# Kernel optimization log

Hardware: AMD Instinct MI355X
Metric: run time of the kernel (lower is better)

## Reference

```python
import jax, jax.numpy as jnp
import numpy as np

NM = 4096; NP = 4096; EM = 65536; EP = 65536; H = 256; HEADS = 4; G = 32


def _lin(k, din, dout):
    k1, k2 = jax.random.split(k)
    return (jax.random.normal(k1, (din, dout), jnp.float32) * (1.0 / np.sqrt(din)),
            jax.random.normal(k2, (dout,), jnp.float32) * 0.01)


def setup_inputs() -> dict:
    key = jax.random.key(0)
    ks = jax.random.split(key, 32)
    inp = {}
    inp['x_mol'] = jax.random.normal(ks[0], (NM, 8), jnp.float32)
    inp['x_prot'] = jax.random.normal(ks[1], (NP, 4), jnp.float32)
    inp['ea_mol'] = jax.random.normal(ks[2], (EM, 2), jnp.float32)
    inp['ea_prot'] = jax.random.normal(ks[3], (EP, 2), jnp.float32)
    inp['ei_mol'] = jax.random.randint(ks[4], (2, EM), 0, NM)
    inp['ei_prot'] = jax.random.randint(ks[5], (2, EP), 0, NP)
    inp['batch_mol'] = jnp.sort(jax.random.randint(ks[6], (NM,), 0, G))
    inp['batch_prot'] = jnp.sort(jax.random.randint(ks[7], (NP,), 0, G))
    inp['node_lin_mol_w'], inp['node_lin_mol_b'] = _lin(ks[8], 8, H)
    inp['node_lin_prot_w'], inp['node_lin_prot_b'] = _lin(ks[9], 4, H)
    inp['edge_lin_mol_w'], inp['edge_lin_mol_b'] = _lin(ks[10], 2, H)
    inp['edge_lin_prot_w'], inp['edge_lin_prot_b'] = _lin(ks[11], 2, H)
    # two GINE conv layers per graph, each with a 2-layer MLP; stack layer dim first
    for pref, base in (('mol', 12), ('prot', 16)):
        w1 = []; b1 = []; w2 = []; b2 = []
        for l in range(2):
            w, b = _lin(ks[base + 2 * l], H, H); w1.append(w); b1.append(b)
            w, b = _lin(ks[base + 2 * l + 1], H, H); w2.append(w); b2.append(b)
        inp[pref + '_w1'] = jnp.stack(w1); inp[pref + '_b1'] = jnp.stack(b1)
        inp[pref + '_w2'] = jnp.stack(w2); inp[pref + '_b2'] = jnp.stack(b2)
    for pref, base in (('mp', 20), ('pm', 23)):
        inp[pref + '_wq'], inp[pref + '_bq'] = _lin(ks[base], H, H)
        inp[pref + '_wk'], inp[pref + '_bk'] = _lin(ks[base + 1], H, H)
        inp[pref + '_wv'], inp[pref + '_bv'] = _lin(ks[base + 2], H, H)
    inp['fc1_w'], inp['fc1_b'] = _lin(ks[26], 2 * H, H)
    inp['fc2_w'], inp['fc2_b'] = _lin(ks[27], H, 1)
    return inp


def _gine_stack(x, ei, e, w1, b1, w2, b2):
    # GINEConv (eps=0): x_i' = relu(nn(x_i + sum_j relu(x_j + e_ji))), 2 layers, shared edge emb
    src, dst = ei[0], ei[1]
    n = x.shape[0]
    for l in range(w1.shape[0]):
        msg = jax.nn.relu(x[src] + e)                      # [E, H]
        agg = jax.ops.segment_sum(msg, dst, num_segments=n)  # [N, H]
        h = x + agg
        h = jax.nn.relu(h @ w1[l] + b1[l]) @ w2[l] + b2[l]
        x = jax.nn.relu(h)
    return x


def _cross_attn(qn, kn, wq, bq, wk, bk, wv, bv):
    nq, d = qn.shape
    nk = kn.shape[0]
    hd = d // HEADS
    Q = (qn @ wq + bq).reshape(nq, HEADS, hd)
    K = (kn @ wk + bk).reshape(nk, HEADS, hd)
    V = (kn @ wv + bv).reshape(nk, HEADS, hd)
    scores = jnp.einsum('qhd,khd->hqk', Q, K) / np.float32(hd ** 0.5)
    w = jax.nn.softmax(scores, axis=-1)
    return jnp.einsum('hqk,khd->qhd', w, V).reshape(nq, d)


def _seg_mean(h, seg, n):
    s = jax.ops.segment_sum(h, seg, num_segments=n)
    c = jax.ops.segment_sum(jnp.ones((h.shape[0], 1), h.dtype), seg, num_segments=n)
    return s / jnp.maximum(c, 1.0)


def reference(x_mol, x_prot, ea_mol, ea_prot, ei_mol, ei_prot, batch_mol, batch_prot,
              node_lin_mol_w, node_lin_mol_b, node_lin_prot_w, node_lin_prot_b,
              edge_lin_mol_w, edge_lin_mol_b, edge_lin_prot_w, edge_lin_prot_b,
              mol_w1, mol_b1, mol_w2, mol_b2, prot_w1, prot_b1, prot_w2, prot_b2,
              mp_wq, mp_bq, mp_wk, mp_bk, mp_wv, mp_bv,
              pm_wq, pm_bq, pm_wk, pm_bk, pm_wv, pm_bv,
              fc1_w, fc1_b, fc2_w, fc2_b):
    hm = x_mol @ node_lin_mol_w + node_lin_mol_b
    hp = x_prot @ node_lin_prot_w + node_lin_prot_b
    em = ea_mol @ edge_lin_mol_w + edge_lin_mol_b
    ep = ea_prot @ edge_lin_prot_w + edge_lin_prot_b
    H_mol = _gine_stack(hm, ei_mol, em, mol_w1, mol_b1, mol_w2, mol_b2)
    H_prot = _gine_stack(hp, ei_prot, ep, prot_w1, prot_b1, prot_w2, prot_b2)
    H_mol_c = H_mol + _cross_attn(H_mol, H_prot, mp_wq, mp_bq, mp_wk, mp_bk, mp_wv, mp_bv)
    H_prot_c = H_prot + _cross_attn(H_prot, H_mol, pm_wq, pm_bq, pm_wk, pm_bk, pm_wv, pm_bv)
    z_mol = _seg_mean(H_mol_c, batch_mol, G)
    z_prot = _seg_mean(H_prot_c, batch_prot, G)
    z = jnp.concatenate([z_mol, z_prot], axis=1)
    x = jax.nn.relu(z @ fc1_w + fc1_b)
    out = jax.nn.sigmoid(x @ fc2_w + fc2_b)
    return out.squeeze(-1)
```

## Files before the change

### kernel.cpp

```cpp
#include <hip/hip_runtime.h>
#include <math.h>

#define HDIM 256
#define NMOL 4096
#define NPROT 4096
#define NEDGE 65536
#define NG 32

typedef _Float16 f16x8 __attribute__((ext_vector_type(8)));
typedef _Float16 f16x4 __attribute__((ext_vector_type(4)));
typedef __attribute__((ext_vector_type(4))) float f32x4;

__device__ __forceinline__ void splitf(float x, _Float16& h, _Float16& l) {
  h = (_Float16)x;
  l = (_Float16)(x - (float)h);
}

struct __align__(16) EdgeRec { int src; float a0; float a1; int pad; };

struct PtrPack { const float* p[14]; };

__global__ __launch_bounds__(256) void k_prep_wt(PtrPack pk, _Float16* __restrict__ dh,
                                                 _Float16* __restrict__ dl) {
  __shared__ float Ts[64][68];
  const int m = blockIdx.z;
  const int n0 = blockIdx.y * 64, k0 = blockIdx.x * 64;
  const float* W = pk.p[m];
  const int t = threadIdx.x;
#pragma unroll
  for (int rep = 0; rep < 16; ++rep) {
    int k = rep * 4 + (t >> 6);
    int n = t & 63;
    Ts[n][k] = W[(size_t)(k0 + k) * 256 + n0 + n];
  }
  __syncthreads();
#pragma unroll
  for (int rep = 0; rep < 2; ++rep) {
    int idx = t + rep * 256;
    int nr = idx >> 3, koff = (idx & 7) * 8;
    f16x8 vh, vl;
#pragma unroll
    for (int i = 0; i < 8; ++i) {
      _Float16 h, l;
      splitf(Ts[nr][koff + i], h, l);
      vh[i] = h; vl[i] = l;
    }
    size_t off = (size_t)m * 65536 + (size_t)(n0 + nr) * 256 + k0 + koff;
    *(f16x8*)&dh[off] = vh;
    *(f16x8*)&dl[off] = vl;
  }
}

struct EmbJob {
  const float* x; const float* w; const float* b;
  _Float16* oh; _Float16* ol; int K;
};

__global__ __launch_bounds__(256) void k_node_embed2(EmbJob j0, EmbJob j1) {
  const EmbJob& j = blockIdx.y ? j1 : j0;
  const int i = blockIdx.x;
  const int c = threadIdx.x;
  float acc = j.b[c];
  for (int k = 0; k < j.K; ++k) acc += j.x[i * j.K + k] * j.w[k * HDIM + c];
  _Float16 h, l;
  splitf(acc, h, l);
  j.oh[(size_t)i * HDIM + c] = h;
  j.ol[(size_t)i * HDIM + c] = l;
}

__global__ __launch_bounds__(1024) void k_csr_all(
    const int* __restrict__ ei0, const int* __restrict__ ei1,
    const float* __restrict__ ea0, const float* __restrict__ ea1,
    int* __restrict__ off0, int* __restrict__ off1,
    EdgeRec* __restrict__ er0, EdgeRec* __restrict__ er1) {
  __shared__ int lcnt[4096];
  __shared__ int wbase[16];
  const int dir = blockIdx.x;
  const int* ei = dir ? ei1 : ei0;
  const float* ea = dir ? ea1 : ea0;
  int* off = dir ? off1 : off0;
  EdgeRec* er = dir ? er1 : er0;
  const int t = threadIdx.x;
  const int lane = t & 63, wv = t >> 6;

#pragma unroll
  for (int i = 0; i < 4; ++i) lcnt[t + i * 1024] = 0;
  __syncthreads();
  for (int e = t; e < NEDGE; e += 1024) atomicAdd(&lcnt[ei[NEDGE + e]], 1);
  __syncthreads();

  int loc[4], s = 0;
#pragma unroll
  for (int i = 0; i < 4; ++i) { loc[i] = lcnt[t * 4 + i]; s += loc[i]; }
  int pre = s;
#pragma unroll
  for (int o = 1; o < 64; o <<= 1) {
    int v = __shfl_up(pre, o, 64);
    if (lane >= o) pre += v;
  }
  if (lane == 63) wbase[wv] = pre;
  __syncthreads();
  if (t == 0) {
    int a = 0;
    for (int i = 0; i < 16; ++i) { int v = wbase[i]; wbase[i] = a; a += v; }
  }
  __syncthreads();
  int a = wbase[wv] + pre - s;
#pragma unroll
  for (int i = 0; i < 4; ++i) {
    off[t * 4 + i] = a;
    lcnt[t * 4 + i] = a;
    a += loc[i];
  }
  if (t == 1023) off[4096] = a;
  __syncthreads();

  for (int e = t; e < NEDGE; e += 1024) {
    int d = ei[NEDGE + e];
    int pos = atomicAdd(&lcnt[d], 1);
    EdgeRec r;
    r.src = ei[e];
    r.a0 = ea[2 * e];
    r.a1 = ea[2 * e + 1];
    r.pad = 0;
    er[pos] = r;
  }
}

struct AggJob {
  const _Float16* xh; const _Float16* xl; const EdgeRec* er;
  const int* off; const float* we; const float* be;
  _Float16* sh; _Float16* sl;
};

__global__ __launch_bounds__(256) void k_agg2(AggJob a0, AggJob a1) {
  const AggJob& a = blockIdx.y ? a1 : a0;
  const int n = blockIdx.x;
  const int c = threadIdx.x;
  const float w0 = a.we[c], w1 = a.we[HDIM + c], bb = a.be[c];
  const int j0 = a.off[n], j1 = a.off[n + 1];
  float sum = 0.f;
  int j = j0;
  for (; j + 1 < j1; j += 2) {
    EdgeRec ra = a.er[j];
    EdgeRec rb = a.er[j + 1];
    float xa = (float)a.xh[(size_t)ra.src * HDIM + c] + (float)a.xl[(size_t)ra.src * HDIM + c];
    float xb = (float)a.xh[(size_t)rb.src * HDIM + c] + (float)a.xl[(size_t)rb.src * HDIM + c];
    sum += fmaxf(xa + ra.a0 * w0 + ra.a1 * w1 + bb, 0.f);
    sum += fmaxf(xb + rb.a0 * w0 + rb.a1 * w1 + bb, 0.f);
  }
  if (j < j1) {
    EdgeRec ra = a.er[j];
    float xa = (float)a.xh[(size_t)ra.src * HDIM + c] + (float)a.xl[(size_t)ra.src * HDIM + c];
    sum += fmaxf(xa + ra.a0 * w0 + ra.a1 * w1 + bb, 0.f);
  }
  float self = (float)a.xh[(size_t)n * HDIM + c] + (float)a.xl[(size_t)n * HDIM + c];
  _Float16 h, l;
  splitf(self + sum, h, l);
  a.sh[(size_t)n * HDIM + c] = h;
  a.sl[(size_t)n * HDIM + c] = l;
}

struct FusedJob {
  const _Float16* Ah; const _Float16* Al;
  const _Float16* W1h; const _Float16* W1l; const float* b1;
  const _Float16* W2h; const _Float16* W2l; const float* b2;
  _Float16* Oh; _Float16* Ol;
};

__global__ __launch_bounds__(256) void k_gine_fused(FusedJob j0, FusedJob j1) {
  const FusedJob J = blockIdx.y ? j1 : j0;
  __shared__ _Float16 Bh[4][64][72], Bl[4][64][72];
  __shared__ _Float16 Ast_h[4][32][72], Ast_l[4][32][72];
  const int t = threadIdx.x;
  const int bm = blockIdx.x * 32;
  const int lane = t & 63, w = t >> 6;
  const int l15 = lane & 15, l4 = lane >> 4;

#pragma unroll
  for (int rep = 0; rep < 4; ++rep) {
    int idx = t + rep * 256;
    int r = idx >> 5;
    int c8 = idx & 31;
    size_t off = (size_t)(bm + r) * 256 + c8 * 8;
    *(f16x8*)&Ast_h[c8 >> 3][r][(c8 & 7) * 8] = *(const f16x8*)&J.Ah[off];
    *(f16x8*)&Ast_l[c8 >> 3][r][(c8 & 7) * 8] = *(const f16x8*)&J.Al[off];
  }
  __syncthreads();

  f32x4 acc[2][4] = {};
  for (int k0 = 0; k0 < 4; ++k0) {
#pragma unroll
    for (int rep = 0; rep < 8; ++rep) {
      int idx = lane + rep * 64;
      int nr = idx >> 3, c8 = idx & 7;
      size_t off = (size_t)(w * 64 + nr) * 256 + k0 * 64 + c8 * 8;
      *(f16x8*)&Bh[w][nr][c8 * 8] = *(const f16x8*)&J.W1h[off];
      *(f16x8*)&Bl[w][nr][c8 * 8] = *(const f16x8*)&J.W1l[off];
    }
#pragma unroll
    for (int kh = 0; kh < 2; ++kh) {
      f16x8 a0h = *(f16x8*)&Ast_h[k0][l15][kh * 32 + l4 * 8];
      f16x8 a0l = *(f16x8*)&Ast_l[k0][l15][kh * 32 + l4 * 8];
      f16x8 a1h = *(f16x8*)&Ast_h[k0][16 + l15][kh * 32 + l4 * 8];
      f16x8 a1l = *(f16x8*)&Ast_l[k0][16 + l15][kh * 32 + l4 * 8];
#pragma unroll
      for (int ni = 0; ni < 4; ++ni) {
        f16x8 bh = *(f16x8*)&Bh[w][ni * 16 + l15][kh * 32 + l4 * 8];
        f16x8 bl = *(f16x8*)&Bl[w][ni * 16 + l15][kh * 32 + l4 * 8];
        acc[0][ni] = __builtin_amdgcn_mfma_f32_16x16x32_f16(a0h, bh, acc[0][ni], 0, 0, 0);
        acc[0][ni] = __builtin_amdgcn_mfma_f32_16x16x32_f16(a0h, bl, acc[0][ni], 0, 0, 0);
        acc[0][ni] = __builtin_amdgcn_mfma_f32_16x16x32_f16(a0l, bh, acc[0][ni], 0, 0, 0);
        acc[1][ni] = __builtin_amdgcn_mfma_f32_16x16x32_f16(a1h, bh, acc[1][ni], 0, 0, 0);
        acc[1][ni] = __builtin_amdgcn_mfma_f32_16x16x32_f16(a1h, bl, acc[1][ni], 0, 0, 0);
        acc[1][ni] = __builtin_amdgcn_mfma_f32_16x16x32_f16(a1l, bh, acc[1][ni], 0, 0, 0);
      }
    }
  }
  __syncthreads();
#pragma unroll
  for (int mi = 0; mi < 2; ++mi)
#pragma unroll
    for (int ni = 0; ni < 4; ++ni) {
      int cl = ni * 16 + l15;
      float bv = J.b1[w * 64 + cl];
#pragma unroll
      for (int r = 0; r < 4; ++r) {
        int row = mi * 16 + l4 * 4 + r;
        float v = fmaxf(acc[mi][ni][r] + bv, 0.f);
        _Float16 hh, ll;
        splitf(v, hh, ll);
        Ast_h[w][row][cl] = hh;
        Ast_l[w][row][cl] = ll;
      }
    }
  __syncthreads();

#pragma unroll
  for (int mi = 0; mi < 2; ++mi)
#pragma unroll
    for (int ni = 0; ni < 4; ++ni) acc[mi][ni] = (f32x4){0.f, 0.f, 0.f, 0.f};
  for (int k0 = 0; k0 < 4; ++k0) {
#pragma unroll
    for (int rep = 0; rep < 8; ++rep) {
      int idx = lane + rep * 64;
      int nr = idx >> 3, c8 = idx & 7;
      size_t off = (size_t)(w * 64 + nr) * 256 + k0 * 64 + c8 * 8;
      *(f16x8*)&Bh[w][nr][c8 * 8] = *(const f16x8*)&J.W2h[off];
      *(f16x8*)&Bl[w][nr][c8 * 8] = *(const f16x8*)&J.W2l[off];
    }
#pragma unroll
    for (int kh = 0; kh < 2; ++kh) {
      f16x8 a0h = *(f16x8*)&Ast_h[k0][l15][kh * 32 + l4 * 8];
      f16x8 a0l = *(f16x8*)&Ast_l[k0][l15][kh * 32 + l4 * 8];
      f16x8 a1h = *(f16x8*)&Ast_h[k0][16 + l15][kh * 32 + l4 * 8];
      f16x8 a1l = *(f16x8*)&Ast_l[k0][16 + l15][kh * 32 + l4 * 8];
#pragma unroll
      for (int ni = 0; ni < 4; ++ni) {
        f16x8 bh = *(f16x8*)&Bh[w][ni * 16 + l15][kh * 32 + l4 * 8];
        f16x8 bl = *(f16x8*)&Bl[w][ni * 16 + l15][kh * 32 + l4 * 8];
        acc[0][ni] = __builtin_amdgcn_mfma_f32_16x16x32_f16(a0h, bh, acc[0][ni], 0, 0, 0);
        acc[0][ni] = __builtin_amdgcn_mfma_f32_16x16x32_f16(a0h, bl, acc[0][ni], 0, 0, 0);
        acc[0][ni] = __builtin_amdgcn_mfma_f32_16x16x32_f16(a0l, bh, acc[0][ni], 0, 0, 0);
        acc[1][ni] = __builtin_amdgcn_mfma_f32_16x16x32_f16(a1h, bh, acc[1][ni], 0, 0, 0);
        acc[1][ni] = __builtin_amdgcn_mfma_f32_16x16x32_f16(a1h, bl, acc[1][ni], 0, 0, 0);
        acc[1][ni] = __builtin_amdgcn_mfma_f32_16x16x32_f16(a1l, bh, acc[1][ni], 0, 0, 0);
      }
    }
  }
#pragma unroll
  for (int mi = 0; mi < 2; ++mi)
#pragma unroll
    for (int ni = 0; ni < 4; ++ni) {
      int col = w * 64 + ni * 16 + l15;
      float bv = J.b2[col];
#pragma unroll
      for (int r = 0; r < 4; ++r) {
        int row = bm + mi * 16 + l4 * 4 + r;
        float v = fmaxf(acc[mi][ni][r] + bv, 0.f);
        _Float16 hh, ll;
        splitf(v, hh, ll);
        J.Oh[(size_t)row * 256 + col] = hh;
        J.Ol[(size_t)row * 256 + col] = ll;
      }
    }
}

struct GJob {
  const _Float16* Ah; const _Float16* Al;
  const _Float16* Bh; const _Float16* Bl;
  const float* bias;
  _Float16* Ch; _Float16* Cl; _Float16* Vt;
  float oscale; int flags;
};
struct GJobs { GJob j[6]; };

__global__ __launch_bounds__(256) void k_gemm(GJobs js) {
  const GJob J = js.j[blockIdx.z];
  const int relu = J.flags & 1;
  const int outmode = J.flags >> 4;
  __shared__ _Float16 Ah[64][72], Al[64][72], Bh[64][72], Bl[64][72];
  const int t = threadIdx.x;
  const int bm = blockIdx.x * 64, bn = blockIdx.y * 64;
  const int lane = t & 63, w = t >> 6;
  const int l15 = lane & 15, l4 = lane >> 4;
  const int wm = (w >> 1) * 32, wn = (w & 1) * 32;
  f32x4 acc[2][2] = {};
  for (int k0 = 0; k0 < 256; k0 += 64) {
    __syncthreads();
#pragma unroll
    for (int rep = 0; rep < 2; ++rep) {
      int idx = t + rep * 256;
      int r = idx >> 3, k8 = (idx & 7) * 8;
      size_t offa = (size_t)(bm + r) * 256 + k0 + k8;
      *(f16x8*)&Ah[r][k8] = *(const f16x8*)&J.Ah[offa];
      *(f16x8*)&Al[r][k8] = *(const f16x8*)&J.Al[offa];
      size_t offb = (size_t)(bn + r) * 256 + k0 + k8;
      *(f16x8*)&Bh[r][k8] = *(const f16x8*)&J.Bh[offb];
      *(f16x8*)&Bl[r][k8] = *(const f16x8*)&J.Bl[offb];
    }
    __syncthreads();
#pragma unroll
    for (int kh = 0; kh < 2; ++kh) {
      f16x8 a0h = *(f16x8*)&Ah[wm + l15][kh * 32 + l4 * 8];
      f16x8 a0l = *(f16x8*)&Al[wm + l15][kh * 32 + l4 * 8];
      f16x8 a1h = *(f16x8*)&Ah[wm + 16 + l15][kh * 32 + l4 * 8];
      f16x8 a1l = *(f16x8*)&Al[wm + 16 + l15][kh * 32 + l4 * 8];
      f16x8 b0h = *(f16x8*)&Bh[wn + l15][kh * 32 + l4 * 8];
      f16x8 b0l = *(f16x8*)&Bl[wn + l15][kh * 32 + l4 * 8];
      f16x8 b1h = *(f16x8*)&Bh[wn + 16 + l15][kh * 32 + l4 * 8];
      f16x8 b1l = *(f16x8*)&Bl[wn + 16 + l15][kh * 32 + l4 * 8];
      acc[0][0] = __builtin_amdgcn_mfma_f32_16x16x32_f16(a0h, b0h, acc[0][0], 0, 0, 0);
      acc[0][0] = __builtin_amdgcn_mfma_f32_16x16x32_f16(a0h, b0l, acc[0][0], 0, 0, 0);
      acc[0][0] = __builtin_amdgcn_mfma_f32_16x16x32_f16(a0l, b0h, acc[0][0], 0, 0, 0);
      acc[0][1] = __builtin_amdgcn_mfma_f32_16x16x32_f16(a0h, b1h, acc[0][1], 0, 0, 0);
      acc[0][1] = __builtin_amdgcn_mfma_f32_16x16x32_f16(a0h, b1l, acc[0][1], 0, 0, 0);
      acc[0][1] = __builtin_amdgcn_mfma_f32_16x16x32_f16(a0l, b1h, acc[0][1], 0, 0, 0);
      acc[1][0] = __builtin_amdgcn_mfma_f32_16x16x32_f16(a1h, b0h, acc[1][0], 0, 0, 0);
      acc[1][0] = __builtin_amdgcn_mfma_f32_16x16x32_f16(a1h, b0l, acc[1][0], 0, 0, 0);
      acc[1][0] = __builtin_amdgcn_mfma_f32_16x16x32_f16(a1l, b0h, acc[1][0], 0, 0, 0);
      acc[1][1] = __builtin_amdgcn_mfma_f32_16x16x32_f16(a1h, b1h, acc[1][1], 0, 0, 0);
      acc[1][1] = __builtin_amdgcn_mfma_f32_16x16x32_f16(a1h, b1l, acc[1][1], 0, 0, 0);
      acc[1][1] = __builtin_amdgcn_mfma_f32_16x16x32_f16(a1l, b1h, acc[1][1], 0, 0, 0);
    }
  }
  if (outmode == 3) __syncthreads();
#pragma unroll
  for (int mi = 0; mi < 2; ++mi)
#pragma unroll
    for (int ni = 0; ni < 2; ++ni) {
      int col = bn + wn + ni * 16 + l15;
      float bv = J.bias[col];
#pragma unroll
      for (int r = 0; r < 4; ++r) {
        int row = bm + wm + mi * 16 + l4 * 4 + r;
        float v = acc[mi][ni][r] + bv;
        if (relu) v = fmaxf(v, 0.f);
        if (outmode == 1) {
          float vs = v * J.oscale;
          _Float16 hh, ll;
          splitf(vs, hh, ll);
          J.Ch[(size_t)row * 256 + col] = hh;
          J.Cl[(size_t)row * 256 + col] = ll;
        } else {
          Ah[wn + ni * 16 + l15][wm + mi * 16 + l4 * 4 + r] = (_Float16)v;
        }
      }
    }
  if (outmode == 3) {
    __syncthreads();
#pragma unroll
    for (int rep = 0; rep < 2; ++rep) {
      int idx = t + rep * 256;
      int d = idx >> 3, n8 = (idx & 7) * 8;
      *(f16x8*)&J.Vt[(size_t)(bn + d) * 4096 + bm + n8] = *(f16x8*)&Ah[d][n8];
    }
  }
}

struct AttnArgs {
  const _Float16* Qh[2]; const _Float16* Ql[2];
  const _Float16* Kh[2]; const _Float16* Kl[2];
  const _Float16* Vth[2];
  _Float16* Opart; float* mpart; float* lpart;
};

__global__ __launch_bounds__(256) void k_attn6(AttnArgs A, int nkq) {
  __shared__ _Float16 Ksh[64][72], Ksl[64][72];
  __shared__ _Float16 Vsh[64][72];
  __shared__ _Float16 Psh[4][32][72];
  const int t = threadIdx.x;
  const int dir = blockIdx.y >> 2, h = blockIdx.y & 3;
  const int q0 = blockIdx.x * 128;
  const int quarter = blockIdx.z;
  const int kbase = quarter * nkq;
  const int lane = t & 63, w = t >> 6;
  const int l15 = lane & 15, l4 = lane >> 4;
  const int qw = q0 + w * 32;

  const _Float16* Qh_g = A.Qh[dir];
  const _Float16* Ql_g = A.Ql[dir];
  const _Float16* Kh_g = A.Kh[dir];
  const _Float16* Kl_g = A.Kl[dir];
  const _Float16* Vth_g = A.Vth[dir];

  f16x8 qh[2][2], ql[2][2];
#pragma unroll
  for (int qf = 0; qf < 2; ++qf) {
    size_t qoff = (size_t)(qw + qf * 16 + l15) * 256 + h * 64;
#pragma unroll
    for (int kh = 0; kh < 2; ++kh) {
      qh[qf][kh] = *(const f16x8*)&Qh_g[qoff + kh * 32 + l4 * 8];
      ql[qf][kh] = *(const f16x8*)&Ql_g[qoff + kh * 32 + l4 * 8];
    }
  }
  f32x4 o[2][4] = {};
  float mrun[2] = {-1e30f, -1e30f};
  float lrun[2] = {0.f, 0.f};

  for (int kt = 0; kt < nkq; kt += 64) {
    const int k0 = kbase + kt;
    __syncthreads();
#pragma unroll
    for (int rep = 0; rep < 2; ++rep) {
      int idx = t + rep * 256;
      int r = idx >> 3, c8 = idx & 7;
      size_t koff = (size_t)(k0 + r) * 256 + h * 64 + c8 * 8;
      *(f16x8*)&Ksh[r][c8 * 8] = *(const f16x8*)&Kh_g[koff];
      *(f16x8*)&Ksl[r][c8 * 8] = *(const f16x8*)&Kl_g[koff];
      int sc = c8 ^ ((r >> 3) & 7);
      size_t voff = (size_t)(h * 64 + r) * 4096 + k0 + c8 * 8;
      *(f16x8*)&Vsh[r][sc * 8] = *(const f16x8*)&Vth_g[voff];
    }
    __syncthreads();

    f32x4 sf[2][4] = {};
#pragma unroll
    for (int kc = 0; kc < 4; ++kc) {
      f16x8 kf0h = *(f16x8*)&Ksh[kc * 16 + l15][l4 * 8];
      f16x8 kf0l = *(f16x8*)&Ksl[kc * 16 + l15][l4 * 8];
      f16x8 kf1h = *(f16x8*)&Ksh[kc * 16 + l15][32 + l4 * 8];
      f16x8 kf1l = *(f16x8*)&Ksl[kc * 16 + l15][32 + l4 * 8];
#pragma unroll
      for (int qf = 0; qf < 2; ++qf) {
        sf[qf][kc] = __builtin_amdgcn_mfma_f32_16x16x32_f16(kf0h, qh[qf][0], sf[qf][kc], 0, 0, 0);
        sf[qf][kc] = __builtin_amdgcn_mfma_f32_16x16x32_f16(kf0h, ql[qf][0], sf[qf][kc], 0, 0, 0);
        sf[qf][kc] = __builtin_amdgcn_mfma_f32_16x16x32_f16(kf0l, qh[qf][0], sf[qf][kc], 0, 0, 0);
        sf[qf][kc] = __builtin_amdgcn_mfma_f32_16x16x32_f16(kf1h, qh[qf][1], sf[qf][kc], 0, 0, 0);
        sf[qf][kc] = __builtin_amdgcn_mfma_f32_16x16x32_f16(kf1h, ql[qf][1], sf[qf][kc], 0, 0, 0);
        sf[qf][kc] = __builtin_amdgcn_mfma_f32_16x16x32_f16(kf1l, qh[qf][1], sf[qf][kc], 0, 0, 0);
      }
    }

#pragma unroll
    for (int qf = 0; qf < 2; ++qf) {
      float mt = -1e30f;
#pragma unroll
      for (int kc = 0; kc < 4; ++kc) {
        float a = fmaxf(fmaxf(sf[qf][kc][0], sf[qf][kc][1]),
                        fmaxf(sf[qf][kc][2], sf[qf][kc][3]));
        mt = fmaxf(mt, a);
      }
      mt = fmaxf(mt, __shfl_xor(mt, 16, 64));
      mt = fmaxf(mt, __shfl_xor(mt, 32, 64));
      float mn = fmaxf(mrun[qf], mt);
      float alpha = __expf(mrun[qf] - mn);
      mrun[qf] = mn;
      float rs = 0.f;
#pragma unroll
      for (int kc = 0; kc < 4; ++kc) {
        float p0 = __expf(sf[qf][kc][0] - mn);
        float p1 = __expf(sf[qf][kc][1] - mn);
        float p2 = __expf(sf[qf][kc][2] - mn);
        float p3 = __expf(sf[qf][kc][3] - mn);
        rs += (p0 + p1) + (p2 + p3);
        f16x4 pv = {(_Float16)p0, (_Float16)p1, (_Float16)p2, (_Float16)p3};
        *(f16x4*)&Psh[w][qf * 16 + l15][kc * 16 + 4 * l4] = pv;
      }
      rs += __shfl_xor(rs, 16, 64);
      rs += __shfl_xor(rs, 32, 64);
      lrun[qf] = lrun[qf] * alpha + rs;
#pragma unroll
      for (int r = 0; r < 4; ++r) {
        float ar = __shfl(alpha, 4 * l4 + r, 64);
        o[qf][0][r] *= ar; o[qf][1][r] *= ar;
        o[qf][2][r] *= ar; o[qf][3][r] *= ar;
      }
    }

#pragma unroll
    for (int kh = 0; kh < 2; ++kh) {
      f16x8 pa0 = *(f16x8*)&Psh[w][l15][kh * 32 + l4 * 8];
      f16x8 pa1 = *(f16x8*)&Psh[w][16 + l15][kh * 32 + l4 * 8];
#pragma unroll
      for (int oc = 0; oc < 4; ++oc) {
        int d = oc * 16 + l15;
        int chunk = (kh * 4 + l4) ^ ((d >> 3) & 7);
        f16x8 vb = *(f16x8*)&Vsh[d][chunk * 8];
        o[0][oc] = __builtin_amdgcn_mfma_f32_16x16x32_f16(pa0, vb, o[0][oc], 0, 0, 0);
        o[1][oc] = __builtin_amdgcn_mfma_f32_16x16x32_f16(pa1, vb, o[1][oc], 0, 0, 0);
      }
    }
  }

  const int slot = dir * 4 + quarter;
#pragma unroll
  for (int qf = 0; qf < 2; ++qf)
#pragma unroll
    for (int oc = 0; oc < 4; ++oc) {
      int col = h * 64 + oc * 16 + l15;
#pragma unroll
      for (int r = 0; r < 4; ++r) {
        int row = qw + qf * 16 + 4 * l4 + r;
        A.Opart[((size_t)slot * 4096 + row) * 256 + col] = (_Float16)o[qf][oc][r];
      }
    }
  if (lane < 16) {
#pragma unroll
    for (int qf = 0; qf < 2; ++qf) {
      int row = qw + qf * 16 + l15;
      A.mpart[(size_t)(slot * 4 + h) * 4096 + row] = mrun[qf];
      A.lpart[(size_t)(slot * 4 + h) * 4096 + row] = lrun[qf];
    }
  }
}

__global__ __launch_bounds__(256) void k_head_all(
    const _Float16* __restrict__ Opart, const float* __restrict__ mpart,
    const float* __restrict__ lpart,
    const _Float16* __restrict__ hmh, const _Float16* __restrict__ hml,
    const _Float16* __restrict__ hph, const _Float16* __restrict__ hpl,
    const int* __restrict__ b_mol, const int* __restrict__ b_prot,
    const float* __restrict__ w1, const float* __restrict__ b1,
    const float* __restrict__ w2, const float* __restrict__ b2,
    float* __restrict__ out) {
  __shared__ float zl[512];
  __shared__ float wsum[4];
  const int g = blockIdx.x;
  const int c = threadIdx.x;
  const int h = c >> 6;
  for (int dir = 0; dir < 2; ++dir) {
    const int* batch = dir ? b_prot : b_mol;
    const _Float16* Hh = dir ? hph : hmh;
    const _Float16* Hl = dir ? hpl : hml;
    int lo = 0, hi = 4096;
    while (lo < hi) { int mid = (lo + hi) >> 1; if (batch[mid] < g) lo = mid + 1; else hi = mid; }
    int start = lo;
    lo = 0; hi = 4096;
    while (lo < hi) { int mid = (lo + hi) >> 1; if (batch[mid] < g + 1) lo = mid + 1; else hi = mid; }
    int end = lo;
    float zacc = 0.f;
    for (int row = start; row < end; ++row) {
      float mv[4], lv[4], M = -1e30f;
#pragma unroll
      for (int q = 0; q < 4; ++q) {
        int slot = dir * 4 + q;
        mv[q] = mpart[(size_t)(slot * 4 + h) * 4096 + row];
        lv[q] = lpart[(size_t)(slot * 4 + h) * 4096 + row];
        M = fmaxf(M, mv[q]);
      }
      float L = 0.f, acc = 0.f;
#pragma unroll
      for (int q = 0; q < 4; ++q) {
        float e = __expf(mv[q] - M);
        L += lv[q] * e;
        acc += (float)Opart[((size_t)(dir * 4 + q) * 4096 + row) * 256 + c] * e;
      }
      float hin = (float)Hh[(size_t)row * 256 + c] + (float)Hl[(size_t)row * 256 + c];
      zacc += acc / L + hin;
    }
    zl[dir * 256 + c] = zacc / fmaxf((float)(end - start), 1.0f);
  }
  __syncthreads();
  float acc = b1[c];
  for (int k = 0; k < 512; ++k) acc += zl[k] * w1[k * HDIM + c];
  acc = fmaxf(acc, 0.f);
  float p = acc * w2[c];
#pragma unroll
  for (int off = 1; off < 64; off <<= 1) p += __shfl_xor(p, off, 64);
  if ((c & 63) == 0) wsum[c >> 6] = p;
  __syncthreads();
  if (c == 0) {
    float s = (wsum[0] + wsum[1]) + (wsum[2] + wsum[3]) + b2[0];
    out[g] = 1.0f / (1.0f + __expf(-s));
  }
}

extern "C" void kernel_launch(void* const* d_in, const int* in_sizes, int n_in,
                              void* d_out, int out_size, void* d_ws, size_t ws_size,
                              hipStream_t stream) {
  const float* x_mol   = (const float*)d_in[0];
  const float* x_prot  = (const float*)d_in[1];
  const float* ea_mol  = (const float*)d_in[2];
  const float* ea_prot = (const float*)d_in[3];
  const int*   ei_mol  = (const int*)d_in[4];
  const int*   ei_prot = (const int*)d_in[5];
  const int*   b_mol   = (const int*)d_in[6];
  const int*   b_prot  = (const int*)d_in[7];
  const float* nlm_w = (const float*)d_in[8];
  const float* nlm_b = (const float*)d_in[9];
  const float* nlp_w = (const float*)d_in[10];
  const float* nlp_b = (const float*)d_in[11];
  const float* elm_w = (const float*)d_in[12];
  const float* elm_b = (const float*)d_in[13];
  const float* elp_w = (const float*)d_in[14];
  const float* elp_b = (const float*)d_in[15];
  const float* mol_w1 = (const float*)d_in[16];
  const float* mol_b1 = (const float*)d_in[17];
  const float* mol_w2 = (const float*)d_in[18];
  const float* mol_b2 = (const float*)d_in[19];
  const float* prot_w1 = (const float*)d_in[20];
  const float* prot_b1 = (const float*)d_in[21];
  const float* prot_w2 = (const float*)d_in[22];
  const float* prot_b2 = (const float*)d_in[23];
  const float* mp_wq = (const float*)d_in[24];
  const float* mp_bq = (const float*)d_in[25];
  const float* mp_wk = (const float*)d_in[26];
  const float* mp_bk = (const float*)d_in[27];
  const float* mp_wv = (const float*)d_in[28];
  const float* mp_bv = (const float*)d_in[29];
  const float* pm_wq = (const float*)d_in[30];
  const float* pm_bq = (const float*)d_in[31];
  const float* pm_wk = (const float*)d_in[32];
  const float* pm_bk = (const float*)d_in[33];
  const float* pm_wv = (const float*)d_in[34];
  const float* pm_bv = (const float*)d_in[35];
  const float* fc1_w = (const float*)d_in[36];
  const float* fc1_b = (const float*)d_in[37];
  const float* fc2_w = (const float*)d_in[38];
  const float* fc2_b = (const float*)d_in[39];
  float* out = (float*)d_out;

  char* W8 = (char*)d_ws;
  const size_t MB = 1u << 20;
  _Float16* wtH  = (_Float16*)(W8 + 0 * MB);
  _Float16* wtL  = (_Float16*)(W8 + 2 * MB);
  _Float16* hmh  = (_Float16*)(W8 + 4 * MB);
  _Float16* hml  = (_Float16*)(W8 + 6 * MB);
  _Float16* hph  = (_Float16*)(W8 + 8 * MB);
  _Float16* hpl  = (_Float16*)(W8 + 10 * MB);
  _Float16* amh  = (_Float16*)(W8 + 12 * MB);
  _Float16* aml  = (_Float16*)(W8 + 14 * MB);
  _Float16* aph  = (_Float16*)(W8 + 16 * MB);
  _Float16* apl  = (_Float16*)(W8 + 18 * MB);
  _Float16* Qh0  = (_Float16*)(W8 + 20 * MB);
  _Float16* Ql0  = (_Float16*)(W8 + 22 * MB);
  _Float16* Kh0  = (_Float16*)(W8 + 24 * MB);
  _Float16* Kl0  = (_Float16*)(W8 + 26 * MB);
  _Float16* Qh1  = (_Float16*)(W8 + 28 * MB);
  _Float16* Ql1  = (_Float16*)(W8 + 30 * MB);
  _Float16* Kh1  = (_Float16*)(W8 + 32 * MB);
  _Float16* Kl1  = (_Float16*)(W8 + 34 * MB);
  _Float16* Vth0 = (_Float16*)(W8 + 36 * MB);
  _Float16* Vth1 = (_Float16*)(W8 + 38 * MB);
  _Float16* Opart = (_Float16*)(W8 + 40 * MB);
  float* mpart = (float*)(W8 + 56 * MB);
  float* lpart = (float*)(W8 + 56 * MB + 512 * 1024);
  int* off_m = (int*)(W8 + 57 * MB);
  int* off_p = off_m + 8192;
  EdgeRec* er_m = (EdgeRec*)(W8 + 58 * MB);
  EdgeRec* er_p = (EdgeRec*)(W8 + 59 * MB);

  PtrPack pk;
  pk.p[0] = mol_w1;           pk.p[1] = mol_w1 + 65536;
  pk.p[2] = mol_w2;           pk.p[3] = mol_w2 + 65536;
  pk.p[4] = prot_w1;          pk.p[5] = prot_w1 + 65536;
  pk.p[6] = prot_w2;          pk.p[7] = prot_w2 + 65536;
  pk.p[8] = mp_wq;  pk.p[9] = mp_wk;  pk.p[10] = mp_wv;
  pk.p[11] = pm_wq; pk.p[12] = pm_wk; pk.p[13] = pm_wv;
  k_prep_wt<<<dim3(4, 4, 14), 256, 0, stream>>>(pk, wtH, wtL);

  k_csr_all<<<2, 1024, 0, stream>>>(ei_mol, ei_prot, ea_mol, ea_prot,
                                    off_m, off_p, er_m, er_p);

  EmbJob em = {x_mol, nlm_w, nlm_b, hmh, hml, 8};
  EmbJob ep = {x_prot, nlp_w, nlp_b, hph, hpl, 4};
  k_node_embed2<<<dim3(NMOL, 2), 256, 0, stream>>>(em, ep);

#define WTH(i) (wtH + (size_t)(i) * 65536)
#define WTL(i) (wtL + (size_t)(i) * 65536)

  AggJob am = {hmh, hml, er_m, off_m, elm_w, elm_b, amh, aml};
  AggJob ap = {hph, hpl, er_p, off_p, elp_w, elp_b, aph, apl};

  for (int l = 0; l < 2; ++l) {
    k_agg2<<<dim3(NMOL, 2), 256, 0, stream>>>(am, ap);
    FusedJob fm = {amh, aml, WTH(l), WTL(l), mol_b1 + l * 256,
                   WTH(2 + l), WTL(2 + l), mol_b2 + l * 256, hmh, hml};
    FusedJob fp = {aph, apl, WTH(4 + l), WTL(4 + l), prot_b1 + l * 256,
                   WTH(6 + l), WTL(6 + l), prot_b2 + l * 256, hph, hpl};
    k_gine_fused<<<dim3(128, 2), 256, 0, stream>>>(fm, fp);
  }

  {
    GJobs q = {};
    q.j[0] = {hmh, hml, WTH(8), WTL(8), mp_bq, Qh0, Ql0, nullptr, 0.125f, 1 << 4};
    q.j[1] = {hph, hpl, WTH(9), WTL(9), mp_bk, Kh0, Kl0, nullptr, 1.0f, 1 << 4};
    q.j[2] = {hph, hpl, WTH(10), WTL(10), mp_bv, nullptr, nullptr, Vth0, 1.0f, 3 << 4};
    q.j[3] = {hph, hpl, WTH(11), WTL(11), pm_bq, Qh1, Ql1, nullptr, 0.125f, 1 << 4};
    q.j[4] = {hmh, hml, WTH(12), WTL(12), pm_bk, Kh1, Kl1, nullptr, 1.0f, 1 << 4};
    q.j[5] = {hmh, hml, WTH(13), WTL(13), pm_bv, nullptr, nullptr, Vth1, 1.0f, 3 << 4};
    k_gemm<<<dim3(64, 4, 6), 256, 0, stream>>>(q);
  }

  AttnArgs aa;
  aa.Qh[0] = Qh0; aa.Ql[0] = Ql0; aa.Kh[0] = Kh0; aa.Kl[0] = Kl0; aa.Vth[0] = Vth0;
  aa.Qh[1] = Qh1; aa.Ql[1] = Ql1; aa.Kh[1] = Kh1; aa.Kl[1] = Kl1; aa.Vth[1] = Vth1;
  aa.Opart = Opart; aa.mpart = mpart; aa.lpart = lpart;
  k_attn6<<<dim3(32, 8, 4), 256, 0, stream>>>(aa, 1024);

  k_head_all<<<NG, 256, 0, stream>>>(Opart, mpart, lpart, hmh, hml, hph, hpl,
                                     b_mol, b_prot, fc1_w, fc1_b, fc2_w, fc2_b, out);
#undef WTH
#undef WTL
}
```

Before: 619.2 us.

## Split head into per-row combine/pool kernel with atomics and small head kernel

The old head kernel ran only 32 blocks, each serially looping over about 128 rows per graph for both directions, which left most of the GPU idle. Now a 8192-block kernel combines the attention partials per row and atomically adds the result into per-graph sums and counts. A separate 32-block kernel then divides by the counts and applies the MLP head. This adds a memset, an extra launch, and float atomics whose summation order is nondeterministic.

```diff
diff --git a/kernel.cpp b/kernel.cpp
--- a/kernel.cpp
+++ b/kernel.cpp
@@ -525,55 +525,54 @@
   }
 }
 
-__global__ __launch_bounds__(256) void k_head_all(
+__global__ __launch_bounds__(256) void k_combine_pool(
     const _Float16* __restrict__ Opart, const float* __restrict__ mpart,
     const float* __restrict__ lpart,
     const _Float16* __restrict__ hmh, const _Float16* __restrict__ hml,
     const _Float16* __restrict__ hph, const _Float16* __restrict__ hpl,
     const int* __restrict__ b_mol, const int* __restrict__ b_prot,
+    float* __restrict__ z, float* __restrict__ cnt) {
+  const int row = blockIdx.x;
+  const int dir = blockIdx.y;
+  const int c = threadIdx.x;
+  const int h = c >> 6;
+  const _Float16* Hh = dir ? hph : hmh;
+  const _Float16* Hl = dir ? hpl : hml;
+  const int g = (dir ? b_prot : b_mol)[row];
+  float mv[4], lv[4], M = -1e30f;
+#pragma unroll
+  for (int q = 0; q < 4; ++q) {
+    int slot = dir * 4 + q;
+    mv[q] = mpart[(size_t)(slot * 4 + h) * 4096 + row];
+    lv[q] = lpart[(size_t)(slot * 4 + h) * 4096 + row];
+    M = fmaxf(M, mv[q]);
+  }
+  float L = 0.f, acc = 0.f;
+#pragma unroll
+  for (int q = 0; q < 4; ++q) {
+    float e = __expf(mv[q] - M);
+    L += lv[q] * e;
+    acc += (float)Opart[((size_t)(dir * 4 + q) * 4096 + row) * 256 + c] * e;
+  }
+  float hin = (float)Hh[(size_t)row * 256 + c] + (float)Hl[(size_t)row * 256 + c];
+  float v = acc / L + hin;
+  atomicAdd(&z[(size_t)g * 512 + dir * 256 + c], v);
+  if (c == 0) atomicAdd(&cnt[dir * 32 + g], 1.0f);
+}
+
+__global__ __launch_bounds__(256) void k_head(
+    const float* __restrict__ z, const float* __restrict__ cnt,
     const float* __restrict__ w1, const float* __restrict__ b1,
     const float* __restrict__ w2, const float* __restrict__ b2,
     float* __restrict__ out) {
-  __shared__ float zl[512];
   __shared__ float wsum[4];
-  const int g = blockIdx.x;
+  const int r = blockIdx.x;
   const int c = threadIdx.x;
-  const int h = c >> 6;
-  for (int dir = 0; dir < 2; ++dir) {
-    const int* batch = dir ? b_prot : b_mol;
-    const _Float16* Hh = dir ? hph : hmh;
-    const _Float16* Hl = dir ? hpl : hml;
-    int lo = 0, hi = 4096;
-    while (lo < hi) { int mid = (lo + hi) >> 1; if (batch[mid] < g) lo = mid + 1; else hi = mid; }
-    int start = lo;
-    lo = 0; hi = 4096;
-    while (lo < hi) { int mid = (lo + hi) >> 1; if (batch[mid] < g + 1) lo = mid + 1; else hi = mid; }
-    int end = lo;
-    float zacc = 0.f;
-    for (int row = start; row < end; ++row) {
-      float mv[4], lv[4], M = -1e30f;
-#pragma unroll
-      for (int q = 0; q < 4; ++q) {
-        int slot = dir * 4 + q;
-        mv[q] = mpart[(size_t)(slot * 4 + h) * 4096 + row];
-        lv[q] = lpart[(size_t)(slot * 4 + h) * 4096 + row];
-        M = fmaxf(M, mv[q]);
-      }
-      float L = 0.f, acc = 0.f;
-#pragma unroll
-      for (int q = 0; q < 4; ++q) {
-        float e = __expf(mv[q] - M);
-        L += lv[q] * e;
-        acc += (float)Opart[((size_t)(dir * 4 + q) * 4096 + row) * 256 + c] * e;
-      }
-      float hin = (float)Hh[(size_t)row * 256 + c] + (float)Hl[(size_t)row * 256 + c];
-      zacc += acc / L + hin;
-    }
-    zl[dir * 256 + c] = zacc / fmaxf((float)(end - start), 1.0f);
-  }
-  __syncthreads();
+  const float im = 1.0f / fmaxf(cnt[r], 1.0f);
+  const float ip = 1.0f / fmaxf(cnt[32 + r], 1.0f);
   float acc = b1[c];
-  for (int k = 0; k < 512; ++k) acc += zl[k] * w1[k * HDIM + c];
+  for (int k = 0; k < 256; ++k) acc += (z[r * 512 + k] * im) * w1[k * HDIM + c];
+  for (int k = 256; k < 512; ++k) acc += (z[r * 512 + k] * ip) * w1[k * HDIM + c];
   acc = fmaxf(acc, 0.f);
   float p = acc * w2[c];
 #pragma unroll
@@ -582,7 +581,7 @@
   __syncthreads();
   if (c == 0) {
     float s = (wsum[0] + wsum[1]) + (wsum[2] + wsum[3]) + b2[0];
-    out[g] = 1.0f / (1.0f + __expf(-s));
+    out[r] = 1.0f / (1.0f + __expf(-s));
   }
 }
 
@@ -658,6 +657,8 @@
   float* lpart = (float*)(W8 + 56 * MB + 512 * 1024);
   int* off_m = (int*)(W8 + 57 * MB);
   int* off_p = off_m + 8192;
+  float* zb  = (float*)(off_p + 8192);
+  float* cnt = zb + 32 * 512;
   EdgeRec* er_m = (EdgeRec*)(W8 + 58 * MB);
   EdgeRec* er_p = (EdgeRec*)(W8 + 59 * MB);
 
@@ -709,8 +710,11 @@
   aa.Opart = Opart; aa.mpart = mpart; aa.lpart = lpart;
   k_attn6<<<dim3(32, 8, 4), 256, 0, stream>>>(aa, 1024);
 
-  k_head_all<<<NG, 256, 0, stream>>>(Opart, mpart, lpart, hmh, hml, hph, hpl,
-                                     b_mol, b_prot, fc1_w, fc1_b, fc2_w, fc2_b, out);
+  hipMemsetAsync(zb, 0, (32 * 512 + 64) * 4, stream);
+  k_combine_pool<<<dim3(4096, 2), 256, 0, stream>>>(Opart, mpart, lpart,
+                                                    hmh, hml, hph, hpl,
+                                                    b_mol, b_prot, zb, cnt);
+  k_head<<<NG, 256, 0, stream>>>(zb, cnt, fc1_w, fc1_b, fc2_w, fc2_b, out);
 #undef WTH
 #undef WTL
 }
```

After: 563.7 us. -9.0%, faster.
